# Optimization experiments

Hardware: AMD Instinct MI355X
Metric: run time of the kernel (lower is better)

## Reference

```python
import jax, jax.numpy as jnp
import numpy as np

DIM = 4096
B, S = 4, 2048


def setup_inputs() -> dict:
    key = jax.random.key(0)
    ks = jax.random.split(key, 6)
    scale = 1.0 / np.sqrt(DIM)  # nn.Linear-style init scale
    return {
        "x": jax.random.normal(ks[0], (B, S, DIM), dtype=jnp.float32),
        "W1": jax.random.normal(ks[1], (DIM, DIM), dtype=jnp.float32) * scale,
        "W2": jax.random.normal(ks[2], (DIM, DIM), dtype=jnp.float32) * scale,
        "W3": jax.random.normal(ks[3], (DIM, DIM), dtype=jnp.float32) * scale,
        "W4": jax.random.normal(ks[4], (DIM, DIM), dtype=jnp.float32) * scale,
        "Wo": jax.random.normal(ks[5], (DIM, DIM), dtype=jnp.float32) * scale,
    }


def reference(x, W1, W2, W3, W4, Wo):
    # nn.Linear(bias=False): y = x @ W.T
    xA = jnp.einsum('bsd,ed->bse', x, W1)
    xB = jnp.einsum('bsd,ed->bse', x, W2)
    xC = jnp.einsum('bsd,ed->bse', x, W3)
    # xA^T @ xB over the sequence axis -> [B, dim, dim]
    sq = jnp.einsum('bsd,bse->bde', xA, xB)
    sq = jax.nn.softmax(sq, axis=-1)
    # xC @ sq -> [B, S, dim]
    xO = jnp.einsum('bsd,bde->bse', xC, sq)
    xO = jax.nn.softmax(xO, axis=-1)
    xO = jax.nn.silu(jnp.einsum('bsd,ed->bse', xO, W4))
    return jnp.einsum('bsd,ed->bse', x + xO, Wo)
```

## Files before the change

kernel.cpp:

```cpp
#include <hip/hip_runtime.h>
#include <hip/hip_bf16.h>
#include <stdint.h>

#define DIM 4096
#define NB 4
#define SEQ 2048

typedef __bf16 bf16_t;
typedef __bf16 bf16x8 __attribute__((ext_vector_type(8)));
typedef float f32x4 __attribute__((ext_vector_type(4)));

__device__ __forceinline__ uint16_t f2bf_u(float f) {
  union { float f; uint32_t u; } v; v.f = f;
  uint32_t r = v.u + 0x7FFFu + ((v.u >> 16) & 1u);
  return (uint16_t)(r >> 16);
}

__global__ __launch_bounds__(256) void cvt_f32_bf16_k(const float* __restrict__ in,
                                                      uint16_t* __restrict__ out, long n) {
  long i = ((long)blockIdx.x * 256 + threadIdx.x) * 8;
  long stride = (long)gridDim.x * 256 * 8;
  for (; i < n; i += stride) {
    float4 a = *(const float4*)(in + i);
    float4 b = *(const float4*)(in + i + 4);
    ushort4 o0 = make_ushort4(f2bf_u(a.x), f2bf_u(a.y), f2bf_u(a.z), f2bf_u(a.w));
    ushort4 o1 = make_ushort4(f2bf_u(b.x), f2bf_u(b.y), f2bf_u(b.z), f2bf_u(b.w));
    *(ushort4*)(out + i) = o0;
    *(ushort4*)(out + i + 4) = o1;
  }
}

__device__ __forceinline__ void gload16(const void* g, void* l) {
  __builtin_amdgcn_global_load_lds(
      (const __attribute__((address_space(1))) void*)g,
      (__attribute__((address_space(3))) void*)l,
      16, 0, 0);
}

#define BARX() do { asm volatile("" ::: "memory"); __builtin_amdgcn_s_barrier(); asm volatile("" ::: "memory"); } while (0)
#define VMW(n) asm volatile("s_waitcnt vmcnt(" #n ")" ::: "memory")

__device__ __forceinline__ void readA(bf16x8 (&fa)[4][2], const char* p, int c0, int c1) {
#pragma unroll
  for (int m = 0; m < 4; ++m) {
    fa[m][0] = *(const bf16x8*)(p + m * 2048 + c0);
    fa[m][1] = *(const bf16x8*)(p + m * 2048 + c1);
  }
}
__device__ __forceinline__ void readB(bf16x8 (&fb)[2][2], const char* p, int c0, int c1) {
#pragma unroll
  for (int n = 0; n < 2; ++n) {
    fb[n][0] = *(const bf16x8*)(p + n * 2048 + c0);
    fb[n][1] = *(const bf16x8*)(p + n * 2048 + c1);
  }
}
__device__ __forceinline__ void mmaQ(f32x4 (&acc)[4][2], const bf16x8 (&fa)[4][2],
                                     const bf16x8 (&fb)[2][2]) {
#pragma unroll
  for (int m = 0; m < 4; ++m)
#pragma unroll
    for (int n = 0; n < 2; ++n)
#pragma unroll
      for (int kk = 0; kk < 2; ++kk)
        acc[m][n] = __builtin_amdgcn_mfma_f32_16x16x32_bf16(fa[m][kk], fb[n][kk], acc[m][n], 0, 0, 0);
}
__device__ __forceinline__ void stageH(const bf16_t* gt, int soff, long rsk, char* lb, int t16) {
  gload16(gt + soff, lb + t16);
  gload16(gt + soff + rsk, lb + 8192 + t16);
}

template <int EPI>
__global__ __launch_bounds__(512, 2) void gemm256(
    const bf16_t* __restrict__ Abase, const bf16_t* __restrict__ Bbase,
    void* __restrict__ Cout, const float* __restrict__ Xadd,
    int M, int N, int K, long sA, long sB, long sC) {
  __shared__ char smem[131072];
  char* As = smem;
  char* Bs = smem + 65536;

  const int tid = threadIdx.x;
  const int lane = tid & 63;
  const int wave = tid >> 6;
  const int wm = wave >> 2;
  const int wn = wave & 3;
  const int lr = lane & 15;
  const int hi = lane >> 4;

  const int nwg = gridDim.x;
  int wg = blockIdx.x;
  if ((nwg & 7) == 0) wg = (wg & 7) * (nwg >> 3) + (wg >> 3);
  const int nbn = N >> 8;
  const int bm = wg / nbn, bn = wg % nbn;

  const bf16_t* A = Abase + (long)blockIdx.y * sA;
  const bf16_t* B = Bbase + (long)blockIdx.y * sB;
  const bf16_t* A0p = A + (long)(bm * 256) * K;
  const bf16_t* A1p = A0p + (long)128 * K;
  const bf16_t* B0p = B + (long)(bn * 256) * K;
  const bf16_t* B1p = B0p + (long)128 * K;
  const long rsk = (long)64 * K;

  const int t16 = tid * 16;
  const int lp = t16 ^ (((t16 >> 7) & 7) << 4);
  const int soff = (lp >> 7) * K + ((lp & 127) >> 1);

  const int swz = (lr & 7) << 4;
  const int c0 = (hi * 16) ^ swz;
  const int c1 = c0 ^ 64;
  const int aR = (wm * 64 + lr) * 128;
  const int bR = (wn * 32 + lr) * 128;

  f32x4 acc[2][2][4][2] = {};
  bf16x8 fa0[4][2], fa1[4][2], fb0[2][2], fb1[2][2];

  stageH(A0p, soff, rsk, As, t16);
  stageH(A1p, soff, rsk, As + 16384, t16);
  stageH(B0p, soff, rsk, Bs, t16);
  stageH(B1p, soff, rsk, Bs + 16384, t16);
  VMW(4);
  stageH(A0p + 64, soff, rsk, As + 32768, t16);
  stageH(A1p + 64, soff, rsk, As + 49152, t16);
  stageH(B0p + 64, soff, rsk, Bs + 32768, t16);
  VMW(6);
  BARX();

  const int NIT = K >> 7;
  for (int i = 0; i < NIT; ++i) {
    const bool last = (i == NIT - 1);
    const int k1 = (2 * i + 1) * 64;
    readA(fa0, As + aR, c0, c1);
    readB(fb0, Bs + bR, c0, c1);
    stageH(B1p + k1, soff, rsk, Bs + 49152, t16);
    BARX();
    __builtin_amdgcn_s_setprio(1); mmaQ(acc[0][0], fa0, fb0); __builtin_amdgcn_s_setprio(0);
    BARX();
    readA(fa1, As + 16384 + aR, c0, c1);
    if (!last) stageH(A0p + k1 + 64, soff, rsk, As, t16);
    BARX();
    __builtin_amdgcn_s_setprio(1); mmaQ(acc[1][0], fa1, fb0); __builtin_amdgcn_s_setprio(0);
    BARX();
    readB(fb1, Bs + 16384 + bR, c0, c1);
    if (!last) stageH(A1p + k1 + 64, soff, rsk, As + 16384, t16);
    BARX();
    __builtin_amdgcn_s_setprio(1); mmaQ(acc[0][1], fa0, fb1); __builtin_amdgcn_s_setprio(0);
    BARX();
    if (!last) stageH(B0p + k1 + 64, soff, rsk, Bs, t16);
    BARX();
    __builtin_amdgcn_s_setprio(1); mmaQ(acc[1][1], fa1, fb1); __builtin_amdgcn_s_setprio(0);
    if (last) { VMW(0); } else { VMW(6); }
    BARX();
    readA(fa0, As + 32768 + aR, c0, c1);
    readB(fb0, Bs + 32768 + bR, c0, c1);
    if (!last) stageH(B1p + k1 + 64, soff, rsk, Bs + 16384, t16);
    BARX();
    __builtin_amdgcn_s_setprio(1); mmaQ(acc[0][0], fa0, fb0); __builtin_amdgcn_s_setprio(0);
    BARX();
    readA(fa1, As + 49152 + aR, c0, c1);
    if (!last) stageH(A0p + k1 + 128, soff, rsk, As + 32768, t16);
    BARX();
    __builtin_amdgcn_s_setprio(1); mmaQ(acc[1][0], fa1, fb0); __builtin_amdgcn_s_setprio(0);
    BARX();
    readB(fb1, Bs + 49152 + bR, c0, c1);
    if (!last) stageH(A1p + k1 + 128, soff, rsk, As + 49152, t16);
    BARX();
    __builtin_amdgcn_s_setprio(1); mmaQ(acc[0][1], fa0, fb1); __builtin_amdgcn_s_setprio(0);
    BARX();
    if (!last) stageH(B0p + k1 + 128, soff, rsk, Bs + 32768, t16);
    BARX();
    __builtin_amdgcn_s_setprio(1); mmaQ(acc[1][1], fa1, fb1); __builtin_amdgcn_s_setprio(0);
    if (!last) VMW(6);
    BARX();
  }

  const long cb = (long)blockIdx.y * sC;
#pragma unroll
  for (int mh = 0; mh < 2; ++mh)
#pragma unroll
    for (int nh = 0; nh < 2; ++nh)
#pragma unroll
      for (int m = 0; m < 4; ++m)
#pragma unroll
        for (int n = 0; n < 2; ++n)
#pragma unroll
          for (int j = 0; j < 4; ++j) {
            const int row = bm * 256 + mh * 128 + wm * 64 + m * 16 + hi * 4 + j;
            const int col = bn * 256 + nh * 128 + wn * 32 + n * 16 + lr;
            const long idx = cb + (long)row * N + col;
            const float vv = acc[mh][nh][m][n][j];
            if constexpr (EPI == 0) {
              ((uint16_t*)Cout)[idx] = f2bf_u(vv);
            } else if constexpr (EPI == 1) {
              ((float*)Cout)[idx] = vv;
            } else {
              const float sl = vv / (1.f + __expf(-vv));
              ((uint16_t*)Cout)[idx] = f2bf_u(Xadd[idx] + sl);
            }
          }
}

__global__ __launch_bounds__(256) void softmax_row4096(const float* __restrict__ in,
                                                       uint16_t* __restrict__ out) {
  const long row = blockIdx.x;
  const float* r = in + row * 4096;
  const int tid = threadIdx.x;
  float v[16];
#pragma unroll
  for (int i = 0; i < 4; ++i) {
    float4 a = *(const float4*)(r + tid * 16 + i * 4);
    v[i * 4 + 0] = a.x; v[i * 4 + 1] = a.y; v[i * 4 + 2] = a.z; v[i * 4 + 3] = a.w;
  }
  float m = v[0];
#pragma unroll
  for (int j = 1; j < 16; ++j) m = fmaxf(m, v[j]);
#pragma unroll
  for (int o = 32; o; o >>= 1) m = fmaxf(m, __shfl_xor(m, o));
  __shared__ float red[8];
  if ((tid & 63) == 0) red[tid >> 6] = m;
  __syncthreads();
  m = fmaxf(fmaxf(red[0], red[1]), fmaxf(red[2], red[3]));
  float s = 0.f;
#pragma unroll
  for (int j = 0; j < 16; ++j) { v[j] = __expf(v[j] - m); s += v[j]; }
#pragma unroll
  for (int o = 32; o; o >>= 1) s += __shfl_xor(s, o);
  if ((tid & 63) == 0) red[4 + (tid >> 6)] = s;
  __syncthreads();
  s = (red[4] + red[5]) + (red[6] + red[7]);
  float inv = 1.f / s;
#pragma unroll
  for (int i = 0; i < 4; ++i) {
    ushort4 u = make_ushort4(f2bf_u(v[i * 4 + 0] * inv), f2bf_u(v[i * 4 + 1] * inv),
                             f2bf_u(v[i * 4 + 2] * inv), f2bf_u(v[i * 4 + 3] * inv));
    *(ushort4*)(out + row * 4096 + tid * 16 + i * 4) = u;
  }
}

__global__ __launch_bounds__(256) void rowstat4096(const float* __restrict__ in,
                                                   float2* __restrict__ stats) {
  const long row = blockIdx.x;
  const float* r = in + row * 4096;
  const int tid = threadIdx.x;
  float v[16];
#pragma unroll
  for (int i = 0; i < 4; ++i) {
    float4 a = *(const float4*)(r + tid * 16 + i * 4);
    v[i * 4 + 0] = a.x; v[i * 4 + 1] = a.y; v[i * 4 + 2] = a.z; v[i * 4 + 3] = a.w;
  }
  float m = v[0];
#pragma unroll
  for (int j = 1; j < 16; ++j) m = fmaxf(m, v[j]);
#pragma unroll
  for (int o = 32; o; o >>= 1) m = fmaxf(m, __shfl_xor(m, o));
  __shared__ float red[8];
  if ((tid & 63) == 0) red[tid >> 6] = m;
  __syncthreads();
  m = fmaxf(fmaxf(red[0], red[1]), fmaxf(red[2], red[3]));
  float s = 0.f;
#pragma unroll
  for (int j = 0; j < 16; ++j) s += __expf(v[j] - m);
#pragma unroll
  for (int o = 32; o; o >>= 1) s += __shfl_xor(s, o);
  if ((tid & 63) == 0) red[4 + (tid >> 6)] = s;
  __syncthreads();
  if (tid == 0) {
    s = (red[4] + red[5]) + (red[6] + red[7]);
    stats[row] = make_float2(m, 1.f / s);
  }
}

__global__ __launch_bounds__(256) void transposeSM(const float* __restrict__ in,
                                                   const float2* __restrict__ stats,
                                                   uint16_t* __restrict__ out) {
  __shared__ uint16_t t[64][68];
  __shared__ float2 st[64];
  const int tid = threadIdx.x;
  const int bx = blockIdx.x, by = blockIdx.y;
  if (tid < 64) st[tid] = stats[by * 64 + tid];
  __syncthreads();
  const int tr = tid >> 4;
  const int tc4 = (tid & 15) * 4;
#pragma unroll
  for (int i = 0; i < 4; ++i) {
    const int r = tr + i * 16;
    const float2 ms = st[r];
    float4 v = *(const float4*)&in[(long)(by * 64 + r) * 4096 + bx * 64 + tc4];
    t[r][tc4 + 0] = f2bf_u(__expf(v.x - ms.x) * ms.y);
    t[r][tc4 + 1] = f2bf_u(__expf(v.y - ms.x) * ms.y);
    t[r][tc4 + 2] = f2bf_u(__expf(v.z - ms.x) * ms.y);
    t[r][tc4 + 3] = f2bf_u(__expf(v.w - ms.x) * ms.y);
  }
  __syncthreads();
#pragma unroll
  for (int i = 0; i < 4; ++i) {
    const int oc = tr + i * 16;
    ushort4 v = make_ushort4(t[tc4 + 0][oc], t[tc4 + 1][oc], t[tc4 + 2][oc], t[tc4 + 3][oc]);
    *(ushort4*)&out[(long)(bx * 64 + oc) * 4096 + by * 64 + tc4] = v;
  }
}

extern "C" void kernel_launch(void* const* d_in, const int* in_sizes, int n_in,
                              void* d_out, int out_size, void* d_ws, size_t ws_size,
                              hipStream_t stream) {
  const float* x  = (const float*)d_in[0];
  const float* W1 = (const float*)d_in[1];
  const float* W2 = (const float*)d_in[2];
  const float* W3 = (const float*)d_in[3];
  const float* W4 = (const float*)d_in[4];
  const float* Wo = (const float*)d_in[5];

  char* ws = (char*)d_ws;
  const long SD  = (long)SEQ * DIM;
  const long BSD = (long)NB * SD;
  const long DD  = (long)DIM * DIM;

  bf16_t* xbf  = (bf16_t*)(ws + 0L);
  bf16_t* xAT  = (bf16_t*)(ws + 67108864L);
  bf16_t* xBT  = (bf16_t*)(ws + 134217728L);
  void*   R3   = (void*)  (ws + 201326592L);
  bf16_t* Wbf  = (bf16_t*)(ws + 268435456L);
  bf16_t* sqmT = (bf16_t*)(ws + 301989888L);
  float2* stats = (float2*)d_out;
  float*  xOraw = (float*)d_out;
  (void)ws_size; (void)in_sizes; (void)n_in; (void)out_size;

  cvt_f32_bf16_k<<<2048, 256, 0, stream>>>(x, (uint16_t*)xbf, BSD);

  cvt_f32_bf16_k<<<2048, 256, 0, stream>>>(W1, (uint16_t*)Wbf, DD);
  gemm256<0><<<dim3(128, 4), 512, 0, stream>>>(Wbf, xbf, (void*)xAT, nullptr,
                                               DIM, SEQ, DIM, 0, SD, SD);
  cvt_f32_bf16_k<<<2048, 256, 0, stream>>>(W2, (uint16_t*)Wbf, DD);
  gemm256<0><<<dim3(128, 4), 512, 0, stream>>>(Wbf, xbf, (void*)xBT, nullptr,
                                               DIM, SEQ, DIM, 0, SD, SD);

  for (int b = 0; b < NB; ++b) {
    gemm256<1><<<dim3(256, 1), 512, 0, stream>>>(xAT + b * SD, xBT + b * SD, R3, nullptr,
                                                 DIM, DIM, SEQ, 0, 0, 0);
    rowstat4096<<<DIM, 256, 0, stream>>>((const float*)R3, stats);
    transposeSM<<<dim3(64, 64), 256, 0, stream>>>((const float*)R3, stats,
                                                  (uint16_t*)(sqmT + b * DD));
  }

  cvt_f32_bf16_k<<<2048, 256, 0, stream>>>(W3, (uint16_t*)Wbf, DD);
  gemm256<0><<<dim3(512, 1), 512, 0, stream>>>(xbf, Wbf, R3, nullptr,
                                               NB * SEQ, DIM, DIM, 0, 0, 0);

  gemm256<1><<<dim3(128, 4), 512, 0, stream>>>((const bf16_t*)R3, sqmT, (void*)xOraw, nullptr,
                                               SEQ, DIM, DIM, SD, DD, SD);
  softmax_row4096<<<NB * SEQ, 256, 0, stream>>>(xOraw, (uint16_t*)xBT);

  cvt_f32_bf16_k<<<2048, 256, 0, stream>>>(W4, (uint16_t*)Wbf, DD);
  gemm256<2><<<dim3(512, 1), 512, 0, stream>>>(xBT, Wbf, (void*)xbf, x,
                                               NB * SEQ, DIM, DIM, 0, 0, 0);

  cvt_f32_bf16_k<<<2048, 256, 0, stream>>>(Wo, (uint16_t*)Wbf, DD);
  gemm256<1><<<dim3(512, 1), 512, 0, stream>>>(xbf, Wbf, d_out, nullptr,
                                               NB * SEQ, DIM, DIM, 0, 0, 0);
}
```

Before: 1.805 ms.

## Reschedule GEMM main loop to prefetch LDS fragments one MMA ahead

Restructures the 256x256 GEMM main loop so each LDS fragment read is issued before the preceding MFMA block rather than immediately ahead of its consumer. The first A/B fragments are loaded before the loop, and the MMA order changes to 00,01,10,11. This cuts the barriers per half-iteration from eight to four, with retuned vmcnt waits. It aims to hide LDS latency and reduce barrier stalls, at the cost of more live fragment registers and a trickier hazard ordering between global staging writes and LDS reads.

```diff
diff --git a/kernel.cpp b/kernel.cpp
--- a/kernel.cpp
+++ b/kernel.cpp
@@ -69,6 +69,9 @@
   gload16(gt + soff + rsk, lb + 8192 + t16);
 }
 
+#define PRIO1() __builtin_amdgcn_s_setprio(1)
+#define PRIO0() __builtin_amdgcn_s_setprio(0)
+
 template <int EPI>
 __global__ __launch_bounds__(512, 2) void gemm256(
     const bf16_t* __restrict__ Abase, const bf16_t* __restrict__ Bbase,
@@ -117,57 +120,54 @@
   stageH(A1p, soff, rsk, As + 16384, t16);
   stageH(B0p, soff, rsk, Bs, t16);
   stageH(B1p, soff, rsk, Bs + 16384, t16);
-  VMW(4);
   stageH(A0p + 64, soff, rsk, As + 32768, t16);
   stageH(A1p + 64, soff, rsk, As + 49152, t16);
   stageH(B0p + 64, soff, rsk, Bs + 32768, t16);
   VMW(6);
   BARX();
+  readA(fa0, As + aR, c0, c1);
+  readB(fb0, Bs + bR, c0, c1);
 
   const int NIT = K >> 7;
   for (int i = 0; i < NIT; ++i) {
     const bool last = (i == NIT - 1);
     const int k1 = (2 * i + 1) * 64;
-    readA(fa0, As + aR, c0, c1);
-    readB(fb0, Bs + bR, c0, c1);
+    readB(fb1, Bs + 16384 + bR, c0, c1);
     stageH(B1p + k1, soff, rsk, Bs + 49152, t16);
-    BARX();
-    __builtin_amdgcn_s_setprio(1); mmaQ(acc[0][0], fa0, fb0); __builtin_amdgcn_s_setprio(0);
+    PRIO1(); mmaQ(acc[0][0], fa0, fb0); PRIO0();
     BARX();
     readA(fa1, As + 16384 + aR, c0, c1);
     if (!last) stageH(A0p + k1 + 64, soff, rsk, As, t16);
-    BARX();
-    __builtin_amdgcn_s_setprio(1); mmaQ(acc[1][0], fa1, fb0); __builtin_amdgcn_s_setprio(0);
-    BARX();
-    readB(fb1, Bs + 16384 + bR, c0, c1);
+    PRIO1(); mmaQ(acc[0][1], fa0, fb1); PRIO0();
+    if (last) { VMW(0); } else { VMW(8); }
+    BARX();
+    readA(fa0, As + 32768 + aR, c0, c1);
     if (!last) stageH(A1p + k1 + 64, soff, rsk, As + 16384, t16);
-    BARX();
-    __builtin_amdgcn_s_setprio(1); mmaQ(acc[0][1], fa0, fb1); __builtin_amdgcn_s_setprio(0);
-    BARX();
+    PRIO1(); mmaQ(acc[1][0], fa1, fb0); PRIO0();
+    if (!last) VMW(6);
+    BARX();
+    readB(fb0, Bs + 32768 + bR, c0, c1);
     if (!last) stageH(B0p + k1 + 64, soff, rsk, Bs, t16);
-    BARX();
-    __builtin_amdgcn_s_setprio(1); mmaQ(acc[1][1], fa1, fb1); __builtin_amdgcn_s_setprio(0);
-    if (last) { VMW(0); } else { VMW(6); }
-    BARX();
-    readA(fa0, As + 32768 + aR, c0, c1);
-    readB(fb0, Bs + 32768 + bR, c0, c1);
+    PRIO1(); mmaQ(acc[1][1], fa1, fb1); PRIO0();
+    if (!last) VMW(6);
+    BARX();
+    readB(fb1, Bs + 49152 + bR, c0, c1);
     if (!last) stageH(B1p + k1 + 64, soff, rsk, Bs + 16384, t16);
-    BARX();
-    __builtin_amdgcn_s_setprio(1); mmaQ(acc[0][0], fa0, fb0); __builtin_amdgcn_s_setprio(0);
+    PRIO1(); mmaQ(acc[0][0], fa0, fb0); PRIO0();
     BARX();
     readA(fa1, As + 49152 + aR, c0, c1);
     if (!last) stageH(A0p + k1 + 128, soff, rsk, As + 32768, t16);
-    BARX();
-    __builtin_amdgcn_s_setprio(1); mmaQ(acc[1][0], fa1, fb0); __builtin_amdgcn_s_setprio(0);
-    BARX();
-    readB(fb1, Bs + 49152 + bR, c0, c1);
+    PRIO1(); mmaQ(acc[0][1], fa0, fb1); PRIO0();
+    if (!last) VMW(8);
+    BARX();
+    if (!last) readA(fa0, As + aR, c0, c1);
     if (!last) stageH(A1p + k1 + 128, soff, rsk, As + 49152, t16);
-    BARX();
-    __builtin_amdgcn_s_setprio(1); mmaQ(acc[0][1], fa0, fb1); __builtin_amdgcn_s_setprio(0);
-    BARX();
+    PRIO1(); mmaQ(acc[1][0], fa1, fb0); PRIO0();
+    if (!last) VMW(6);
+    BARX();
+    if (!last) readB(fb0, Bs + bR, c0, c1);
     if (!last) stageH(B0p + k1 + 128, soff, rsk, Bs + 32768, t16);
-    BARX();
-    __builtin_amdgcn_s_setprio(1); mmaQ(acc[1][1], fa1, fb1); __builtin_amdgcn_s_setprio(0);
+    PRIO1(); mmaQ(acc[1][1], fa1, fb1); PRIO0();
     if (!last) VMW(6);
     BARX();
   }
```

New measurement: 2.593 ms. +43.6%, slower.
